# Kernel optimization log

Hardware: AMD Instinct MI355X
Metric: run time of the kernel (lower is better)

## Reference

```python
import jax, jax.numpy as jnp
import numpy as np

N = 50000      # total atoms in batched graph
E = 800000     # edges
IN = 128       # in_feats
OUT = 64       # out_feats (per GAT head)
H = 4          # num_heads
NEG_SLOPE = 0.2
BN_EPS = 1e-5


def setup_inputs() -> dict:
    key = jax.random.key(0)
    ks = jax.random.split(key, 16)
    s = 0.1  # keep activations well-scaled
    return {
        "node_feats": jax.random.normal(ks[0], (N, IN), jnp.float32),
        "W_fc":       jax.random.normal(ks[1], (IN, H * OUT), jnp.float32) * s,
        "attn_l":     jax.random.normal(ks[2], (H, OUT), jnp.float32) * s,
        "attn_r":     jax.random.normal(ks[3], (H, OUT), jnp.float32) * s,
        "gat_res_w":  jax.random.normal(ks[4], (IN, H * OUT), jnp.float32) * s,
        "gat_bias":   jax.random.normal(ks[5], (H * OUT,), jnp.float32) * s,
        "conv_w":     jax.random.normal(ks[6], (1, H, 1), jnp.float32) * s,
        "conv_b":     jax.random.normal(ks[7], (1,), jnp.float32) * s,
        "res_w":      jax.random.normal(ks[8], (IN, OUT), jnp.float32) * s,
        "res_b":      jax.random.normal(ks[9], (OUT,), jnp.float32) * s,
        "bn_gamma":   jnp.ones((OUT,), jnp.float32),
        "bn_beta":    jnp.zeros((OUT,), jnp.float32),
        "src":        jax.random.randint(ks[10], (E,), 0, N, jnp.int32),
        "dst":        jax.random.randint(ks[11], (E,), 0, N, jnp.int32),
        "etype":      0,
    }


def reference(node_feats, W_fc, attn_l, attn_r, gat_res_w, gat_bias,
              conv_w, conv_b, res_w, res_b, bn_gamma, bn_beta,
              src, dst, etype):
    # ---- GATConv (DGL semantics, eval mode: no dropout) ----
    h = (node_feats @ W_fc).reshape(-1, H, OUT)            # [N,H,D]
    el = jnp.sum(h * attn_l, axis=-1)                      # [N,H]
    er = jnp.sum(h * attn_r, axis=-1)                      # [N,H]
    e = jax.nn.leaky_relu(el[src] + er[dst], NEG_SLOPE)    # [E,H]
    # segment softmax over incoming edges of each dst node
    m = jax.ops.segment_max(e, dst, num_segments=N)        # [N,H]
    m = jnp.where(jnp.isfinite(m), m, 0.0)                 # empty segments
    a = jnp.exp(e - m[dst])                                # [E,H]
    ssum = jax.ops.segment_sum(a, dst, num_segments=N)     # [N,H]
    alpha = a / (ssum[dst] + 1e-16)                        # [E,H]
    # weighted aggregation: rst[v] = sum_{(u->v)} alpha * h[u]
    rst = jax.ops.segment_sum(alpha[:, :, None] * h[src], dst, num_segments=N)  # [N,H,D]
    # GAT residual (in != H*OUT -> linear res_fc, no bias) + bias + activation
    rst = rst + (node_feats @ gat_res_w).reshape(-1, H, OUT) + gat_bias.reshape(H, OUT)
    rst = jax.nn.relu(rst)                                 # [N,H,D]
    # ---- Conv1d(4 -> 1, kernel=1): weighted head merge ----
    y = jnp.einsum("nhd,h->nd", rst, conv_w[0, :, 0]) + conv_b[0]  # [N,D]
    # ---- outer residual ----
    y = y + jax.nn.relu(node_feats @ res_w + res_b)
    # ---- BatchNorm1d (training-style batch stats) ----
    mean = jnp.mean(y, axis=0)
    var = jnp.var(y, axis=0)
    return (y - mean) / jnp.sqrt(var + BN_EPS) * bn_gamma + bn_beta
```

## Files before the change

### kernel.cpp

```cpp
#include <hip/hip_runtime.h>

#define IN_F   128
#define OUTD   64
#define HOUT   256
#define NEG_SLOPE 0.2f
#define BN_EPS 1e-5f
#define HISTB  256

typedef __attribute__((ext_vector_type(8))) short bf16x8;
typedef __attribute__((ext_vector_type(4))) float f32x4;
typedef __attribute__((ext_vector_type(2))) float f32x2;

__device__ __forceinline__ unsigned short f2bf(float f) {
    union { float f; unsigned u; } v; v.f = f;
    unsigned r = (v.u + 0x7FFF + ((v.u >> 16) & 1)) >> 16;
    return (unsigned short)r;
}
__device__ __forceinline__ float bf2f(unsigned short h) {
    union { unsigned u; float f; } v; v.u = ((unsigned)h) << 16;
    return v.f;
}
__device__ __forceinline__ float u2f(unsigned u) {
    union { unsigned u; float f; } v; v.u = u;
    return v.f;
}
__device__ __forceinline__ unsigned f2u(float f) {
    union { float f; unsigned u; } v; v.f = f;
    return v.u;
}

__device__ __forceinline__ int b2idx(int c, int k) {
    int tt, j;
    if (c < 256)      { tt = (c >> 4) & 3;                     j = c >> 6; }
    else if (c < 512) { int cc = c - 256; tt = 4 + ((cc >> 4) & 3); j = cc >> 6; }
    else if (c < 576) { int cc = c - 512; tt = 8;              j = cc >> 4; }
    else              { tt = 9;                                j = 0; }
    int n15 = c & 15;
    int ks = k >> 5, qd = (k >> 3) & 3, kk = k & 7;
    return ((((tt * 4 + j) * 4 + ks) * 64) + qd * 16 + n15) * 8 + kk;
}

__global__ __launch_bounds__(256) void k0_pack(
    const float* __restrict__ W_fc, const float* __restrict__ W_gres,
    const float* __restrict__ W_res,
    const float* __restrict__ attn_l, const float* __restrict__ attn_r,
    unsigned short* __restrict__ Btg2)
{
    int bid = blockIdx.x, t = threadIdx.x;
    if (bid < 288) {
        int idx = bid * 256 + t;
        int c = idx >> 7, k = idx & 127;
        float v;
        if (c < 256)      v = W_fc[k * HOUT + c];
        else if (c < 512) v = W_gres[k * HOUT + (c - 256)];
        else              v = W_res[k * OUTD + (c - 512)];
        Btg2[b2idx(c, k)] = f2bf(v);
        return;
    }
    for (int p = t; p < 512; p += 256) {
        int h = p >> 7, k = p & 127;
        float sl = 0.f, sr = 0.f;
        for (int d = 0; d < 64; ++d) {
            float wv = W_fc[k * HOUT + h * 64 + d];
            sl += wv * attn_l[h * 64 + d];
            sr += wv * attn_r[h * 64 + d];
        }
        Btg2[b2idx(576 + h, k)] = f2bf(sl);
        Btg2[b2idx(580 + h, k)] = f2bf(sr);
    }
    for (int p = t; p < 8 * 128; p += 256) {
        int c = 584 + (p >> 7), k = p & 127;
        Btg2[b2idx(c, k)] = 0;
    }
}

__global__ __launch_bounds__(256) void k1_gemm(
    const float* __restrict__ A, const unsigned short* __restrict__ Btg2,
    const float* __restrict__ gat_bias, const float* __restrict__ res_b,
    const int* __restrict__ dst, int* __restrict__ degree, int* __restrict__ rank,
    unsigned char* __restrict__ Hh8, unsigned char* __restrict__ Hr8,
    unsigned short* __restrict__ Rres,
    float* __restrict__ el, float* __restrict__ er,
    int N, int E, int Gblocks)
{
    int t = threadIdx.x;

    if (blockIdx.x >= Gblocks) {
        int ht = (blockIdx.x - Gblocks) * 256 + t;
        for (int e = ht; e < E; e += HISTB * 256)
            rank[e] = atomicAdd(degree + dst[e], 1);
        return;
    }

    int w = t >> 6, lane = t & 63, quad = lane >> 4, n15 = lane & 15;
    int gw = blockIdx.x * 4 + w;
    int T = (N + 15) / 16;
    if (gw >= T) return;

    int m0 = gw * 16;
    bool full = (m0 + 16 <= N);
    int lofs = (quad * 16 + n15) * 8;

    bf16x8 af[4];
    {
        int r = m0 + n15;
#pragma unroll
        for (int ks = 0; ks < 4; ++ks) {
            float4 v0 = make_float4(0.f, 0.f, 0.f, 0.f), v1 = v0;
            if (r < N) {
                const float* ap = A + (size_t)r * IN_F + ks * 32 + quad * 8;
                v0 = *(const float4*)ap;
                v1 = *(const float4*)(ap + 4);
            }
            bf16x8 o;
            o[0] = f2bf(v0.x); o[1] = f2bf(v0.y); o[2] = f2bf(v0.z); o[3] = f2bf(v0.w);
            o[4] = f2bf(v1.x); o[5] = f2bf(v1.y); o[6] = f2bf(v1.z); o[7] = f2bf(v1.w);
            af[ks] = o;
        }
    }

#pragma unroll
    for (int s = 0; s < 4; ++s) {
        f32x4 acc[4] = {};
#pragma unroll
        for (int ks = 0; ks < 4; ++ks) {
            bf16x8 bfr[4];
#pragma unroll
            for (int j = 0; j < 4; ++j)
                bfr[j] = *(const bf16x8*)(Btg2 + ((s * 16 + j * 4 + ks) << 9) + lofs);
#pragma unroll
            for (int j = 0; j < 4; ++j)
                acc[j] = __builtin_amdgcn_mfma_f32_16x16x32_bf16(af[ks], bfr[j], acc[j], 0, 0, 0);
        }
#pragma unroll
        for (int reg = 0; reg < 4; ++reg) {
            int r = m0 + quad * 4 + reg;
            if (full || r < N) {
                unsigned pk = (unsigned)__builtin_amdgcn_cvt_pk_fp8_f32(acc[0][reg], acc[1][reg], 0, false);
                pk = (unsigned)__builtin_amdgcn_cvt_pk_fp8_f32(acc[2][reg], acc[3][reg], (int)pk, true);
                *(unsigned*)(Hh8 + ((size_t)r << 8) + (s * 16 + n15) * 4) = pk;
            }
        }
    }

#pragma unroll
    for (int s = 0; s < 4; ++s) {
        f32x4 acc[4] = {};
#pragma unroll
        for (int ks = 0; ks < 4; ++ks) {
            bf16x8 bfr[4];
#pragma unroll
            for (int j = 0; j < 4; ++j)
                bfr[j] = *(const bf16x8*)(Btg2 + (((4 + s) * 16 + j * 4 + ks) << 9) + lofs);
#pragma unroll
            for (int j = 0; j < 4; ++j)
                acc[j] = __builtin_amdgcn_mfma_f32_16x16x32_bf16(af[ks], bfr[j], acc[j], 0, 0, 0);
        }
        float b0 = gat_bias[0 * 64 + s * 16 + n15];
        float b1 = gat_bias[1 * 64 + s * 16 + n15];
        float b2 = gat_bias[2 * 64 + s * 16 + n15];
        float b3 = gat_bias[3 * 64 + s * 16 + n15];
#pragma unroll
        for (int reg = 0; reg < 4; ++reg) {
            int r = m0 + quad * 4 + reg;
            if (full || r < N) {
                unsigned pk = (unsigned)__builtin_amdgcn_cvt_pk_fp8_f32(acc[0][reg] + b0, acc[1][reg] + b1, 0, false);
                pk = (unsigned)__builtin_amdgcn_cvt_pk_fp8_f32(acc[2][reg] + b2, acc[3][reg] + b3, (int)pk, true);
                *(unsigned*)(Hr8 + ((size_t)r << 8) + (s * 16 + n15) * 4) = pk;
            }
        }
    }

    {
        f32x4 acc[4] = {};
#pragma unroll
        for (int ks = 0; ks < 4; ++ks) {
            bf16x8 bfr[4];
#pragma unroll
            for (int j = 0; j < 4; ++j)
                bfr[j] = *(const bf16x8*)(Btg2 + ((8 * 16 + j * 4 + ks) << 9) + lofs);
#pragma unroll
            for (int j = 0; j < 4; ++j)
                acc[j] = __builtin_amdgcn_mfma_f32_16x16x32_bf16(af[ks], bfr[j], acc[j], 0, 0, 0);
        }
#pragma unroll
        for (int reg = 0; reg < 4; ++reg) {
            int r = m0 + quad * 4 + reg;
            if (full || r < N) {
#pragma unroll
                for (int j = 0; j < 4; ++j)
                    Rres[(size_t)r * OUTD + j * 16 + n15] = f2bf(acc[j][reg] + res_b[j * 16 + n15]);
            }
        }
    }

    {
        f32x4 acc2 = {};
#pragma unroll
        for (int ks = 0; ks < 4; ++ks) {
            bf16x8 b = *(const bf16x8*)(Btg2 + ((9 * 16 + ks) << 9) + lofs);
            acc2 = __builtin_amdgcn_mfma_f32_16x16x32_bf16(af[ks], b, acc2, 0, 0, 0);
        }
#pragma unroll
        for (int reg = 0; reg < 4; ++reg) {
            int r = m0 + quad * 4 + reg;
            if ((full || r < N) && n15 < 8) {
                float v = acc2[reg];
                if (n15 < 4) el[(size_t)r * 4 + n15] = v;
                else         er[(size_t)r * 4 + (n15 - 4)] = v;
            }
        }
    }
}

__global__ __launch_bounds__(256) void scanA_kernel(const int* __restrict__ degree,
                                                    int* __restrict__ excl,
                                                    int* __restrict__ blocksum, int N) {
    __shared__ int sm[256];
    int t = threadIdx.x;
    int i = blockIdx.x * 256 + t;
    int d = (i < N) ? degree[i] : 0;
    sm[t] = d; __syncthreads();
    for (int off = 1; off < 256; off <<= 1) {
        int v = (t >= off) ? sm[t - off] : 0;
        __syncthreads();
        sm[t] += v;
        __syncthreads();
    }
    if (i < N) excl[i] = sm[t] - d;
    if (t == 255) blocksum[blockIdx.x] = sm[255];
}

__global__ __launch_bounds__(256) void scatter_kernel(
    const int* __restrict__ src, const int* __restrict__ dst,
    const int* __restrict__ rank, const int* __restrict__ excl,
    const int* __restrict__ blocksum, int* __restrict__ base,
    unsigned* __restrict__ usrc_sorted, int E, int nb) {
    __shared__ int sm[256];
    __shared__ int base_lds[256];
    int t = threadIdx.x;
    int d0 = (t < nb) ? blocksum[t] : 0;
    sm[t] = d0; __syncthreads();
    for (int off = 1; off < 256; off <<= 1) {
        int v = (t >= off) ? sm[t - off] : 0;
        __syncthreads();
        sm[t] += v;
        __syncthreads();
    }
    base_lds[t] = sm[t] - d0;
    if (blockIdx.x == 0) base[t] = sm[t] - d0;
    __syncthreads();

    int e = blockIdx.x * 256 + t;
    if (e >= E) return;
    int d = dst[e];
    int p = excl[d] + base_lds[d >> 8] + rank[e];
    usrc_sorted[p] = (unsigned)src[e] << 8;
}

__global__ __launch_bounds__(256) void agg_kernel(
    const unsigned char* __restrict__ Hh8, const unsigned char* __restrict__ Hr8,
    const unsigned short* __restrict__ Rres, const float* __restrict__ el,
    const float* __restrict__ er,
    const int* __restrict__ excl, const int* __restrict__ base,
    const unsigned* __restrict__ usrc_sorted,
    const float* __restrict__ conv_w, const float* __restrict__ conv_b,
    float* __restrict__ y, float* __restrict__ bnsum8, float* __restrict__ bnsq8,
    int N, int E)
{
    __shared__ float smem[256];
    __shared__ float smem2[256];
    int t = threadIdx.x;
    int wave = t >> 6, lane = t & 63;
    int v = blockIdx.x * 4 + wave;

    float yv = 0.f;
    if (v < N) {
        int b  = excl[v] + base[v >> 8];
        int e2 = (v + 1 < N) ? (excl[v + 1] + base[(v + 1) >> 8]) : E;
        int deg = e2 - b;

        float4 rv = *(const float4*)(er + (size_t)v * 4);
        const unsigned char* hbase = Hh8 + lane * 4;
        float a0 = 0.f, a1 = 0.f, a2 = 0.f, a3 = 0.f;
        float p0 = 0.f, p1 = 0.f, p2 = 0.f, p3 = 0.f;

        for (int i0 = 0; i0 < deg; i0 += 64) {
            int j = i0 + lane;
            unsigned ux = 0;
            float s0 = 0.f, s1 = 0.f, s2 = 0.f, s3 = 0.f;
            if (j < deg) {
                ux = usrc_sorted[b + j];
                float4 l = *(const float4*)(el + ((size_t)(ux >> 8)) * 4);
                float x;
                x = l.x + rv.x; x = x > 0.f ? x : NEG_SLOPE * x; s0 = __expf(x);
                x = l.y + rv.y; x = x > 0.f ? x : NEG_SLOPE * x; s1 = __expf(x);
                x = l.z + rv.z; x = x > 0.f ? x : NEG_SLOPE * x; s2 = __expf(x);
                x = l.w + rv.w; x = x > 0.f ? x : NEG_SLOPE * x; s3 = __expf(x);
                p0 += s0; p1 += s1; p2 += s2; p3 += s3;
            }
            int cl = deg - i0; if (cl > 64) cl = 64;
            int jj = 0;
            for (; jj + 3 < cl; jj += 4) {
                unsigned u_[4], hv[4];
                float w0[4], w1[4], w2[4], w3[4];
#pragma unroll
                for (int k = 0; k < 4; ++k) {
                    u_[k] = (unsigned)__builtin_amdgcn_readlane((int)ux, jj + k);
                    w0[k] = u2f((unsigned)__builtin_amdgcn_readlane((int)f2u(s0), jj + k));
                    w1[k] = u2f((unsigned)__builtin_amdgcn_readlane((int)f2u(s1), jj + k));
                    w2[k] = u2f((unsigned)__builtin_amdgcn_readlane((int)f2u(s2), jj + k));
                    w3[k] = u2f((unsigned)__builtin_amdgcn_readlane((int)f2u(s3), jj + k));
                }
#pragma unroll
                for (int k = 0; k < 4; ++k)
                    hv[k] = *(const unsigned*)(hbase + u_[k]);
#pragma unroll
                for (int k = 0; k < 4; ++k) {
                    f32x2 lo = __builtin_amdgcn_cvt_pk_f32_fp8(hv[k], false);
                    f32x2 hi = __builtin_amdgcn_cvt_pk_f32_fp8(hv[k], true);
                    a0 += w0[k] * lo.x;
                    a1 += w1[k] * lo.y;
                    a2 += w2[k] * hi.x;
                    a3 += w3[k] * hi.y;
                }
            }
            for (; jj < cl; ++jj) {
                unsigned uA = (unsigned)__builtin_amdgcn_readlane((int)ux, jj);
                float w0 = u2f((unsigned)__builtin_amdgcn_readlane((int)f2u(s0), jj));
                float w1 = u2f((unsigned)__builtin_amdgcn_readlane((int)f2u(s1), jj));
                float w2 = u2f((unsigned)__builtin_amdgcn_readlane((int)f2u(s2), jj));
                float w3 = u2f((unsigned)__builtin_amdgcn_readlane((int)f2u(s3), jj));
                unsigned hvA = *(const unsigned*)(hbase + uA);
                f32x2 lo = __builtin_amdgcn_cvt_pk_f32_fp8(hvA, false);
                f32x2 hi = __builtin_amdgcn_cvt_pk_f32_fp8(hvA, true);
                a0 += w0 * lo.x;
                a1 += w1 * lo.y;
                a2 += w2 * hi.x;
                a3 += w3 * hi.y;
            }
        }
#pragma unroll
        for (int off = 1; off < 64; off <<= 1) {
            p0 += __shfl_xor(p0, off); p1 += __shfl_xor(p1, off);
            p2 += __shfl_xor(p2, off); p3 += __shfl_xor(p3, off);
        }
        float r0 = 1.f / (p0 + 1e-16f), r1 = 1.f / (p1 + 1e-16f);
        float r2 = 1.f / (p2 + 1e-16f), r3 = 1.f / (p3 + 1e-16f);

        unsigned hr = *(const unsigned*)(Hr8 + ((size_t)v << 8) + lane * 4);
        f32x2 rlo = __builtin_amdgcn_cvt_pk_f32_fp8(hr, false);
        f32x2 rhi = __builtin_amdgcn_cvt_pk_f32_fp8(hr, true);
        float resv = bf2f(Rres[(size_t)v * OUTD + lane]);
        yv = conv_b[0] + (resv > 0.f ? resv : 0.f);
        float tt;
        tt = a0 * r0 + rlo.x; tt = tt > 0.f ? tt : 0.f; yv += conv_w[0] * tt;
        tt = a1 * r1 + rlo.y; tt = tt > 0.f ? tt : 0.f; yv += conv_w[1] * tt;
        tt = a2 * r2 + rhi.x; tt = tt > 0.f ? tt : 0.f; yv += conv_w[2] * tt;
        tt = a3 * r3 + rhi.y; tt = tt > 0.f ? tt : 0.f; yv += conv_w[3] * tt;
        y[(size_t)v * OUTD + lane] = yv;
    }

    smem[t] = yv;
    smem2[t] = yv * yv;
    __syncthreads();
    if (t < 64) {
        float s = smem[t] + smem[t + 64] + smem[t + 128] + smem[t + 192];
        float q = smem2[t] + smem2[t + 64] + smem2[t + 128] + smem2[t + 192];
        int c = (blockIdx.x & 7) << 6;
        atomicAdd(bnsum8 + c + t, s);
        atomicAdd(bnsq8 + c + t, q);
    }
}

__global__ __launch_bounds__(256) void norm_kernel(
    const float* __restrict__ y,
    const float* __restrict__ bnsum8, const float* __restrict__ bnsq8,
    const float* __restrict__ gamma, const float* __restrict__ beta,
    float* __restrict__ out, int total4, float invN) {
    __shared__ float scale[64], shift[64];
    int t = threadIdx.x;
    if (t < 64) {
        float s = 0.f, q = 0.f;
#pragma unroll
        for (int c = 0; c < 8; ++c) { s += bnsum8[c * 64 + t]; q += bnsq8[c * 64 + t]; }
        float mean = s * invN;
        float var = q * invN - mean * mean;
        float sc = gamma[t] * rsqrtf(var + BN_EPS);
        scale[t] = sc;
        shift[t] = beta[t] - mean * sc;
    }
    __syncthreads();
    int idx = blockIdx.x * blockDim.x + t;
    if (idx >= total4) return;
    float4 v = *(const float4*)(y + (size_t)idx * 4);
    int d = (idx * 4) & 63;
    float4 o;
    o.x = v.x * scale[d + 0] + shift[d + 0];
    o.y = v.y * scale[d + 1] + shift[d + 1];
    o.z = v.z * scale[d + 2] + shift[d + 2];
    o.w = v.w * scale[d + 3] + shift[d + 3];
    *(float4*)(out + (size_t)idx * 4) = o;
}

extern "C" void kernel_launch(void* const* d_in, const int* in_sizes, int n_in,
                              void* d_out, int out_size, void* d_ws, size_t ws_size,
                              hipStream_t stream) {
    const float* node_feats = (const float*)d_in[0];
    const float* W_fc       = (const float*)d_in[1];
    const float* attn_l     = (const float*)d_in[2];
    const float* attn_r     = (const float*)d_in[3];
    const float* gat_res_w  = (const float*)d_in[4];
    const float* gat_bias   = (const float*)d_in[5];
    const float* conv_w     = (const float*)d_in[6];
    const float* conv_b     = (const float*)d_in[7];
    const float* res_w      = (const float*)d_in[8];
    const float* res_b      = (const float*)d_in[9];
    const float* bn_gamma   = (const float*)d_in[10];
    const float* bn_beta    = (const float*)d_in[11];
    const int*   src        = (const int*)d_in[12];
    const int*   dst        = (const int*)d_in[13];

    const int N = in_sizes[0] / IN_F;
    const int E = in_sizes[12];
    const int nb = (N + 255) / 256;
    const int T = (N + 15) / 16;
    const int Gblocks = (T + 3) / 4;

    char* ws = (char*)d_ws;
    size_t off = 0;
    auto alloc = [&](size_t bytes) -> void* {
        void* p = (void*)(ws + off);
        off += (bytes + 255) & ~(size_t)255;
        return p;
    };

    int*   degree  = (int*)alloc((size_t)N * 4);
    float* bnsum8  = (float*)alloc(8 * 64 * 4);
    float* bnsq8   = (float*)alloc(8 * 64 * 4);
    size_t zero_bytes = off;
    int*            rank        = (int*)alloc((size_t)E * 4);
    int*            excl        = (int*)alloc((size_t)N * 4);
    int*            blocksum    = (int*)alloc(256 * 4);
    int*            base        = (int*)alloc(256 * 4);
    unsigned*       usrc_sorted = (unsigned*)alloc((size_t)E * 4);
    unsigned short* Btg2        = (unsigned short*)alloc((size_t)10 * 16 * 512 * 2);
    unsigned char*  Hh8         = (unsigned char*)alloc((size_t)N * 256);
    unsigned char*  Hr8         = (unsigned char*)alloc((size_t)N * 256);
    unsigned short* Rres        = (unsigned short*)alloc((size_t)N * OUTD * 2);
    float*          el          = (float*)alloc((size_t)N * 4 * 4);
    float*          er          = (float*)alloc((size_t)N * 4 * 4);
    float*          y           = (float*)alloc((size_t)N * OUTD * 4);
    (void)ws_size; (void)n_in; (void)out_size;

    hipMemsetAsync(d_ws, 0, zero_bytes, stream);

    k0_pack<<<289, 256, 0, stream>>>(W_fc, gat_res_w, res_w, attn_l, attn_r, Btg2);
    k1_gemm<<<Gblocks + HISTB, 256, 0, stream>>>(node_feats, Btg2, gat_bias, res_b,
                                                 dst, degree, rank, Hh8, Hr8, Rres,
                                                 el, er, N, E, Gblocks);
    scanA_kernel<<<nb, 256, 0, stream>>>(degree, excl, blocksum, N);
    scatter_kernel<<<(E + 255) / 256, 256, 0, stream>>>(src, dst, rank, excl, blocksum,
                                                        base, usrc_sorted, E, nb);
    agg_kernel<<<(N + 3) / 4, 256, 0, stream>>>(Hh8, Hr8, Rres, el, er, excl, base,
                                                usrc_sorted, conv_w, conv_b, y,
                                                bnsum8, bnsq8, N, E);
    norm_kernel<<<(N * OUTD / 4 + 255) / 256, 256, 0, stream>>>(y, bnsum8, bnsq8,
                                                                bn_gamma, bn_beta, (float*)d_out,
                                                                N * OUTD / 4, 1.f / (float)N);
}
```

Baseline: 222.2 us.

## Move degree histogram into pack kernel and fuse scatter into GEMM launch

The degree-histogram atomics move from the GEMM kernel into the weight-pack kernel. The scan now runs before the GEMM, so the edge scatter (CSR fill) can run as extra blocks of the GEMM launch instead of as a separate kernel. This removes one launch and overlaps the scatter's memory traffic with the MFMA work. The GEMM inner loops also load all B fragments for a stripe before issuing the MFMAs, which raises register use for more memory-level parallelism.

```diff
diff --git a/kernel.cpp b/kernel.cpp
--- a/kernel.cpp
+++ b/kernel.cpp
@@ -5,7 +5,8 @@
 #define HOUT   256
 #define NEG_SLOPE 0.2f
 #define BN_EPS 1e-5f
-#define HISTB  256
+#define HB     1024
+#define SB     512
 
 typedef __attribute__((ext_vector_type(8))) short bf16x8;
 typedef __attribute__((ext_vector_type(4))) float f32x4;
@@ -44,7 +45,9 @@
     const float* __restrict__ W_fc, const float* __restrict__ W_gres,
     const float* __restrict__ W_res,
     const float* __restrict__ attn_l, const float* __restrict__ attn_r,
-    unsigned short* __restrict__ Btg2)
+    unsigned short* __restrict__ Btg2,
+    const int* __restrict__ dst, int* __restrict__ degree,
+    int* __restrict__ rank, int E)
 {
     int bid = blockIdx.x, t = threadIdx.x;
     if (bid < 288) {
@@ -57,38 +60,63 @@
         Btg2[b2idx(c, k)] = f2bf(v);
         return;
     }
-    for (int p = t; p < 512; p += 256) {
-        int h = p >> 7, k = p & 127;
-        float sl = 0.f, sr = 0.f;
-        for (int d = 0; d < 64; ++d) {
-            float wv = W_fc[k * HOUT + h * 64 + d];
-            sl += wv * attn_l[h * 64 + d];
-            sr += wv * attn_r[h * 64 + d];
-        }
-        Btg2[b2idx(576 + h, k)] = f2bf(sl);
-        Btg2[b2idx(580 + h, k)] = f2bf(sr);
-    }
-    for (int p = t; p < 8 * 128; p += 256) {
-        int c = 584 + (p >> 7), k = p & 127;
-        Btg2[b2idx(c, k)] = 0;
-    }
+    if (bid == 288) {
+        for (int p = t; p < 512; p += 256) {
+            int h = p >> 7, k = p & 127;
+            float sl = 0.f, sr = 0.f;
+            for (int d = 0; d < 64; ++d) {
+                float wv = W_fc[k * HOUT + h * 64 + d];
+                sl += wv * attn_l[h * 64 + d];
+                sr += wv * attn_r[h * 64 + d];
+            }
+            Btg2[b2idx(576 + h, k)] = f2bf(sl);
+            Btg2[b2idx(580 + h, k)] = f2bf(sr);
+        }
+        for (int p = t; p < 8 * 128; p += 256) {
+            int c = 584 + (p >> 7), k = p & 127;
+            Btg2[b2idx(c, k)] = 0;
+        }
+        return;
+    }
+    int ht = (bid - 289) * 256 + t;
+    for (int e = ht; e < E; e += HB * 256)
+        rank[e] = atomicAdd(degree + dst[e], 1);
 }
 
 __global__ __launch_bounds__(256) void k1_gemm(
     const float* __restrict__ A, const unsigned short* __restrict__ Btg2,
     const float* __restrict__ gat_bias, const float* __restrict__ res_b,
-    const int* __restrict__ dst, int* __restrict__ degree, int* __restrict__ rank,
+    const int* __restrict__ src, const int* __restrict__ dst,
+    const int* __restrict__ rank, const int* __restrict__ excl,
+    const int* __restrict__ blocksum, int* __restrict__ base,
+    unsigned* __restrict__ usrc_sorted,
     unsigned char* __restrict__ Hh8, unsigned char* __restrict__ Hr8,
     unsigned short* __restrict__ Rres,
     float* __restrict__ el, float* __restrict__ er,
-    int N, int E, int Gblocks)
+    int N, int E, int Gblocks, int nb)
 {
     int t = threadIdx.x;
 
     if (blockIdx.x >= Gblocks) {
-        int ht = (blockIdx.x - Gblocks) * 256 + t;
-        for (int e = ht; e < E; e += HISTB * 256)
-            rank[e] = atomicAdd(degree + dst[e], 1);
+        __shared__ int sm[256];
+        __shared__ int base_lds[256];
+        int sb = blockIdx.x - Gblocks;
+        int d0 = (t < nb) ? blocksum[t] : 0;
+        sm[t] = d0; __syncthreads();
+        for (int off = 1; off < 256; off <<= 1) {
+            int v = (t >= off) ? sm[t - off] : 0;
+            __syncthreads();
+            sm[t] += v;
+            __syncthreads();
+        }
+        base_lds[t] = sm[t] - d0;
+        if (sb == 0) base[t] = sm[t] - d0;
+        __syncthreads();
+        for (int e = sb * 256 + t; e < E; e += SB * 256) {
+            int d = dst[e];
+            int p = excl[d] + base_lds[d >> 8] + rank[e];
+            usrc_sorted[p] = (unsigned)src[e] << 8;
+        }
         return;
     }
 
@@ -121,17 +149,18 @@
 
 #pragma unroll
     for (int s = 0; s < 4; ++s) {
+        bf16x8 bfr[4][4];
+#pragma unroll
+        for (int ks = 0; ks < 4; ++ks)
+#pragma unroll
+            for (int j = 0; j < 4; ++j)
+                bfr[ks][j] = *(const bf16x8*)(Btg2 + ((s * 16 + j * 4 + ks) << 9) + lofs);
         f32x4 acc[4] = {};
 #pragma unroll
-        for (int ks = 0; ks < 4; ++ks) {
-            bf16x8 bfr[4];
-#pragma unroll
-            for (int j = 0; j < 4; ++j)
-                bfr[j] = *(const bf16x8*)(Btg2 + ((s * 16 + j * 4 + ks) << 9) + lofs);
-#pragma unroll
-            for (int j = 0; j < 4; ++j)
-                acc[j] = __builtin_amdgcn_mfma_f32_16x16x32_bf16(af[ks], bfr[j], acc[j], 0, 0, 0);
-        }
+        for (int ks = 0; ks < 4; ++ks)
+#pragma unroll
+            for (int j = 0; j < 4; ++j)
+                acc[j] = __builtin_amdgcn_mfma_f32_16x16x32_bf16(af[ks], bfr[ks][j], acc[j], 0, 0, 0);
 #pragma unroll
         for (int reg = 0; reg < 4; ++reg) {
             int r = m0 + quad * 4 + reg;
@@ -145,17 +174,18 @@
 
 #pragma unroll
     for (int s = 0; s < 4; ++s) {
+        bf16x8 bfr[4][4];
+#pragma unroll
+        for (int ks = 0; ks < 4; ++ks)
+#pragma unroll
+            for (int j = 0; j < 4; ++j)
+                bfr[ks][j] = *(const bf16x8*)(Btg2 + (((4 + s) * 16 + j * 4 + ks) << 9) + lofs);
         f32x4 acc[4] = {};
 #pragma unroll
-        for (int ks = 0; ks < 4; ++ks) {
-            bf16x8 bfr[4];
-#pragma unroll
-            for (int j = 0; j < 4; ++j)
-                bfr[j] = *(const bf16x8*)(Btg2 + (((4 + s) * 16 + j * 4 + ks) << 9) + lofs);
-#pragma unroll
-            for (int j = 0; j < 4; ++j)
-                acc[j] = __builtin_amdgcn_mfma_f32_16x16x32_bf16(af[ks], bfr[j], acc[j], 0, 0, 0);
-        }
+        for (int ks = 0; ks < 4; ++ks)
+#pragma unroll
+            for (int j = 0; j < 4; ++j)
+                acc[j] = __builtin_amdgcn_mfma_f32_16x16x32_bf16(af[ks], bfr[ks][j], acc[j], 0, 0, 0);
         float b0 = gat_bias[0 * 64 + s * 16 + n15];
         float b1 = gat_bias[1 * 64 + s * 16 + n15];
         float b2 = gat_bias[2 * 64 + s * 16 + n15];
@@ -172,17 +202,18 @@
     }
 
     {
+        bf16x8 bfr[4][4];
+#pragma unroll
+        for (int ks = 0; ks < 4; ++ks)
+#pragma unroll
+            for (int j = 0; j < 4; ++j)
+                bfr[ks][j] = *(const bf16x8*)(Btg2 + ((8 * 16 + j * 4 + ks) << 9) + lofs);
         f32x4 acc[4] = {};
 #pragma unroll
-        for (int ks = 0; ks < 4; ++ks) {
-            bf16x8 bfr[4];
-#pragma unroll
-            for (int j = 0; j < 4; ++j)
-                bfr[j] = *(const bf16x8*)(Btg2 + ((8 * 16 + j * 4 + ks) << 9) + lofs);
-#pragma unroll
-            for (int j = 0; j < 4; ++j)
-                acc[j] = __builtin_amdgcn_mfma_f32_16x16x32_bf16(af[ks], bfr[j], acc[j], 0, 0, 0);
-        }
+        for (int ks = 0; ks < 4; ++ks)
+#pragma unroll
+            for (int j = 0; j < 4; ++j)
+                acc[j] = __builtin_amdgcn_mfma_f32_16x16x32_bf16(af[ks], bfr[ks][j], acc[j], 0, 0, 0);
 #pragma unroll
         for (int reg = 0; reg < 4; ++reg) {
             int r = m0 + quad * 4 + reg;
@@ -195,12 +226,14 @@
     }
 
     {
+        bf16x8 b4[4];
+#pragma unroll
+        for (int ks = 0; ks < 4; ++ks)
+            b4[ks] = *(const bf16x8*)(Btg2 + ((9 * 16 + ks) << 9) + lofs);
         f32x4 acc2 = {};
 #pragma unroll
-        for (int ks = 0; ks < 4; ++ks) {
-            bf16x8 b = *(const bf16x8*)(Btg2 + ((9 * 16 + ks) << 9) + lofs);
-            acc2 = __builtin_amdgcn_mfma_f32_16x16x32_bf16(af[ks], b, acc2, 0, 0, 0);
-        }
+        for (int ks = 0; ks < 4; ++ks)
+            acc2 = __builtin_amdgcn_mfma_f32_16x16x32_bf16(af[ks], b4[ks], acc2, 0, 0, 0);
 #pragma unroll
         for (int reg = 0; reg < 4; ++reg) {
             int r = m0 + quad * 4 + reg;
@@ -229,33 +262,6 @@
     }
     if (i < N) excl[i] = sm[t] - d;
     if (t == 255) blocksum[blockIdx.x] = sm[255];
-}
-
-__global__ __launch_bounds__(256) void scatter_kernel(
-    const int* __restrict__ src, const int* __restrict__ dst,
-    const int* __restrict__ rank, const int* __restrict__ excl,
-    const int* __restrict__ blocksum, int* __restrict__ base,
-    unsigned* __restrict__ usrc_sorted, int E, int nb) {
-    __shared__ int sm[256];
-    __shared__ int base_lds[256];
-    int t = threadIdx.x;
-    int d0 = (t < nb) ? blocksum[t] : 0;
-    sm[t] = d0; __syncthreads();
-    for (int off = 1; off < 256; off <<= 1) {
-        int v = (t >= off) ? sm[t - off] : 0;
-        __syncthreads();
-        sm[t] += v;
-        __syncthreads();
-    }
-    base_lds[t] = sm[t] - d0;
-    if (blockIdx.x == 0) base[t] = sm[t] - d0;
-    __syncthreads();
-
-    int e = blockIdx.x * 256 + t;
-    if (e >= E) return;
-    int d = dst[e];
-    int p = excl[d] + base_lds[d >> 8] + rank[e];
-    usrc_sorted[p] = (unsigned)src[e] << 8;
 }
 
 __global__ __launch_bounds__(256) void agg_kernel(
@@ -455,13 +461,13 @@
 
     hipMemsetAsync(d_ws, 0, zero_bytes, stream);
 
-    k0_pack<<<289, 256, 0, stream>>>(W_fc, gat_res_w, res_w, attn_l, attn_r, Btg2);
-    k1_gemm<<<Gblocks + HISTB, 256, 0, stream>>>(node_feats, Btg2, gat_bias, res_b,
-                                                 dst, degree, rank, Hh8, Hr8, Rres,
-                                                 el, er, N, E, Gblocks);
+    k0_pack<<<289 + HB, 256, 0, stream>>>(W_fc, gat_res_w, res_w, attn_l, attn_r, Btg2,
+                                          dst, degree, rank, E);
     scanA_kernel<<<nb, 256, 0, stream>>>(degree, excl, blocksum, N);
-    scatter_kernel<<<(E + 255) / 256, 256, 0, stream>>>(src, dst, rank, excl, blocksum,
-                                                        base, usrc_sorted, E, nb);
+    k1_gemm<<<Gblocks + SB, 256, 0, stream>>>(node_feats, Btg2, gat_bias, res_b,
+                                              src, dst, rank, excl, blocksum, base,
+                                              usrc_sorted, Hh8, Hr8, Rres,
+                                              el, er, N, E, Gblocks, nb);
     agg_kernel<<<(N + 3) / 4, 256, 0, stream>>>(Hh8, Hr8, Rres, el, er, excl, base,
                                                 usrc_sorted, conv_w, conv_b, y,
                                                 bnsum8, bnsq8, N, E);
```

New measurement: 226.9 us. 2.1% more time.

## Stage GEMM weight tiles in LDS with double buffering and 64-row warp tiles

Applied to the files above, without the earlier changes.

The node-feature GEMM kernel now gives each warp 64 rows (four 16-row MFMA tiles) instead of 16, so every B fragment read is reused across four A tiles. The weight matrix is copied into a double-buffered shared-memory tile with global_load_lds, and the next 16 KB tile is prefetched while the current one feeds the MFMAs. This is meant to cut repeated global and L2 reads of the packed weights. In exchange the GEMM launches about a quarter as many blocks, which lowers parallelism on a wide GPU. Every block, including the histogram blocks, now reserves 32 KB of LDS, and the last staged tile reads a full 16 KB that may extend past the packed weight data.

```diff
diff --git a/kernel.cpp b/kernel.cpp
--- a/kernel.cpp
+++ b/kernel.cpp
@@ -27,6 +27,13 @@
 __device__ __forceinline__ unsigned f2u(float f) {
     union { float f; unsigned u; } v; v.f = f;
     return v.u;
+}
+
+__device__ __forceinline__ void stage16(const void* g, void* l) {
+    __builtin_amdgcn_global_load_lds(
+        (const __attribute__((address_space(1))) unsigned int*)g,
+        (__attribute__((address_space(3))) unsigned int*)l,
+        16, 0, 0);
 }
 
 __device__ __forceinline__ int b2idx(int c, int k) {
@@ -83,6 +90,7 @@
     float* __restrict__ el, float* __restrict__ er,
     int N, int E, int Gblocks)
 {
+    __shared__ short ldsB[2][8192];
     int t = threadIdx.x;
 
     if (blockIdx.x >= Gblocks) {
@@ -93,123 +101,122 @@
     }
 
     int w = t >> 6, lane = t & 63, quad = lane >> 4, n15 = lane & 15;
-    int gw = blockIdx.x * 4 + w;
-    int T = (N + 15) / 16;
-    if (gw >= T) return;
-
-    int m0 = gw * 16;
-    bool full = (m0 + 16 <= N);
-    int lofs = (quad * 16 + n15) * 8;
-
-    bf16x8 af[4];
+    int base = blockIdx.x * 256 + w * 64;
+    bool active = (base < N);
+    int lofs2 = (quad * 16 + n15) * 16;
+
+    bf16x8 af[4][4];
+    if (active) {
+#pragma unroll
+        for (int mi = 0; mi < 4; ++mi) {
+            int r = base + mi * 16 + n15;
+#pragma unroll
+            for (int ks = 0; ks < 4; ++ks) {
+                float4 v0 = make_float4(0.f, 0.f, 0.f, 0.f), v1 = v0;
+                if (r < N) {
+                    const float* ap = A + (size_t)r * IN_F + ks * 32 + quad * 8;
+                    v0 = *(const float4*)ap;
+                    v1 = *(const float4*)(ap + 4);
+                }
+                bf16x8 o;
+                o[0] = f2bf(v0.x); o[1] = f2bf(v0.y); o[2] = f2bf(v0.z); o[3] = f2bf(v0.w);
+                o[4] = f2bf(v1.x); o[5] = f2bf(v1.y); o[6] = f2bf(v1.z); o[7] = f2bf(v1.w);
+                af[mi][ks] = o;
+            }
+        }
+    }
+
     {
-        int r = m0 + n15;
-#pragma unroll
-        for (int ks = 0; ks < 4; ++ks) {
-            float4 v0 = make_float4(0.f, 0.f, 0.f, 0.f), v1 = v0;
-            if (r < N) {
-                const float* ap = A + (size_t)r * IN_F + ks * 32 + quad * 8;
-                v0 = *(const float4*)ap;
-                v1 = *(const float4*)(ap + 4);
-            }
-            bf16x8 o;
-            o[0] = f2bf(v0.x); o[1] = f2bf(v0.y); o[2] = f2bf(v0.z); o[3] = f2bf(v0.w);
-            o[4] = f2bf(v1.x); o[5] = f2bf(v1.y); o[6] = f2bf(v1.z); o[7] = f2bf(v1.w);
-            af[ks] = o;
-        }
-    }
-
-#pragma unroll
-    for (int s = 0; s < 4; ++s) {
-        f32x4 acc[4] = {};
-#pragma unroll
-        for (int ks = 0; ks < 4; ++ks) {
-            bf16x8 bfr[4];
-#pragma unroll
-            for (int j = 0; j < 4; ++j)
-                bfr[j] = *(const bf16x8*)(Btg2 + ((s * 16 + j * 4 + ks) << 9) + lofs);
-#pragma unroll
-            for (int j = 0; j < 4; ++j)
-                acc[j] = __builtin_amdgcn_mfma_f32_16x16x32_bf16(af[ks], bfr[j], acc[j], 0, 0, 0);
-        }
-#pragma unroll
-        for (int reg = 0; reg < 4; ++reg) {
-            int r = m0 + quad * 4 + reg;
-            if (full || r < N) {
-                unsigned pk = (unsigned)__builtin_amdgcn_cvt_pk_fp8_f32(acc[0][reg], acc[1][reg], 0, false);
-                pk = (unsigned)__builtin_amdgcn_cvt_pk_fp8_f32(acc[2][reg], acc[3][reg], (int)pk, true);
-                *(unsigned*)(Hh8 + ((size_t)r << 8) + (s * 16 + n15) * 4) = pk;
-            }
-        }
-    }
-
-#pragma unroll
-    for (int s = 0; s < 4; ++s) {
-        f32x4 acc[4] = {};
-#pragma unroll
-        for (int ks = 0; ks < 4; ++ks) {
-            bf16x8 bfr[4];
-#pragma unroll
-            for (int j = 0; j < 4; ++j)
-                bfr[j] = *(const bf16x8*)(Btg2 + (((4 + s) * 16 + j * 4 + ks) << 9) + lofs);
-#pragma unroll
-            for (int j = 0; j < 4; ++j)
-                acc[j] = __builtin_amdgcn_mfma_f32_16x16x32_bf16(af[ks], bfr[j], acc[j], 0, 0, 0);
-        }
-        float b0 = gat_bias[0 * 64 + s * 16 + n15];
-        float b1 = gat_bias[1 * 64 + s * 16 + n15];
-        float b2 = gat_bias[2 * 64 + s * 16 + n15];
-        float b3 = gat_bias[3 * 64 + s * 16 + n15];
-#pragma unroll
-        for (int reg = 0; reg < 4; ++reg) {
-            int r = m0 + quad * 4 + reg;
-            if (full || r < N) {
-                unsigned pk = (unsigned)__builtin_amdgcn_cvt_pk_fp8_f32(acc[0][reg] + b0, acc[1][reg] + b1, 0, false);
-                pk = (unsigned)__builtin_amdgcn_cvt_pk_fp8_f32(acc[2][reg] + b2, acc[3][reg] + b3, (int)pk, true);
-                *(unsigned*)(Hr8 + ((size_t)r << 8) + (s * 16 + n15) * 4) = pk;
-            }
-        }
-    }
-
-    {
-        f32x4 acc[4] = {};
-#pragma unroll
-        for (int ks = 0; ks < 4; ++ks) {
-            bf16x8 bfr[4];
-#pragma unroll
-            for (int j = 0; j < 4; ++j)
-                bfr[j] = *(const bf16x8*)(Btg2 + ((8 * 16 + j * 4 + ks) << 9) + lofs);
-#pragma unroll
-            for (int j = 0; j < 4; ++j)
-                acc[j] = __builtin_amdgcn_mfma_f32_16x16x32_bf16(af[ks], bfr[j], acc[j], 0, 0, 0);
-        }
-#pragma unroll
-        for (int reg = 0; reg < 4; ++reg) {
-            int r = m0 + quad * 4 + reg;
-            if (full || r < N) {
-#pragma unroll
-                for (int j = 0; j < 4; ++j)
-                    Rres[(size_t)r * OUTD + j * 16 + n15] = f2bf(acc[j][reg] + res_b[j * 16 + n15]);
-            }
-        }
-    }
-
-    {
-        f32x4 acc2 = {};
-#pragma unroll
-        for (int ks = 0; ks < 4; ++ks) {
-            bf16x8 b = *(const bf16x8*)(Btg2 + ((9 * 16 + ks) << 9) + lofs);
-            acc2 = __builtin_amdgcn_mfma_f32_16x16x32_bf16(af[ks], b, acc2, 0, 0, 0);
-        }
-#pragma unroll
-        for (int reg = 0; reg < 4; ++reg) {
-            int r = m0 + quad * 4 + reg;
-            if ((full || r < N) && n15 < 8) {
-                float v = acc2[reg];
-                if (n15 < 4) el[(size_t)r * 4 + n15] = v;
-                else         er[(size_t)r * 4 + (n15 - 4)] = v;
-            }
-        }
+        const char* gb = (const char*)Btg2;
+#pragma unroll
+        for (int c = 0; c < 4; ++c) {
+            int ch = w * 4 + c;
+            stage16(gb + ch * 1024 + lane * 16, (char*)&ldsB[0][0] + ch * 1024);
+        }
+    }
+    __syncthreads();
+
+    for (int tt = 0; tt < 10; ++tt) {
+        int cur = tt & 1;
+        if (tt + 1 < 10) {
+            const char* gb = (const char*)Btg2 + (size_t)(tt + 1) * 16384;
+#pragma unroll
+            for (int c = 0; c < 4; ++c) {
+                int ch = w * 4 + c;
+                stage16(gb + ch * 1024 + lane * 16, (char*)&ldsB[cur ^ 1][0] + ch * 1024);
+            }
+        }
+        if (active) {
+            f32x4 acc[4][4] = {};
+#pragma unroll
+            for (int j = 0; j < 4; ++j) {
+                bf16x8 bj[4];
+#pragma unroll
+                for (int ks = 0; ks < 4; ++ks)
+                    bj[ks] = *(const bf16x8*)((const char*)&ldsB[cur][0] + (j * 4 + ks) * 1024 + lofs2);
+#pragma unroll
+                for (int ks = 0; ks < 4; ++ks)
+#pragma unroll
+                    for (int mi = 0; mi < 4; ++mi)
+                        acc[mi][j] = __builtin_amdgcn_mfma_f32_16x16x32_bf16(af[mi][ks], bj[ks], acc[mi][j], 0, 0, 0);
+            }
+            if (tt < 4) {
+                int s = tt;
+#pragma unroll
+                for (int mi = 0; mi < 4; ++mi)
+#pragma unroll
+                    for (int reg = 0; reg < 4; ++reg) {
+                        int r = base + mi * 16 + quad * 4 + reg;
+                        if (r < N) {
+                            unsigned pk = (unsigned)__builtin_amdgcn_cvt_pk_fp8_f32(acc[mi][0][reg], acc[mi][1][reg], 0, false);
+                            pk = (unsigned)__builtin_amdgcn_cvt_pk_fp8_f32(acc[mi][2][reg], acc[mi][3][reg], (int)pk, true);
+                            *(unsigned*)(Hh8 + ((size_t)r << 8) + (s * 16 + n15) * 4) = pk;
+                        }
+                    }
+            } else if (tt < 8) {
+                int s = tt - 4;
+                float b0 = gat_bias[0 * 64 + s * 16 + n15];
+                float b1 = gat_bias[1 * 64 + s * 16 + n15];
+                float b2 = gat_bias[2 * 64 + s * 16 + n15];
+                float b3 = gat_bias[3 * 64 + s * 16 + n15];
+#pragma unroll
+                for (int mi = 0; mi < 4; ++mi)
+#pragma unroll
+                    for (int reg = 0; reg < 4; ++reg) {
+                        int r = base + mi * 16 + quad * 4 + reg;
+                        if (r < N) {
+                            unsigned pk = (unsigned)__builtin_amdgcn_cvt_pk_fp8_f32(acc[mi][0][reg] + b0, acc[mi][1][reg] + b1, 0, false);
+                            pk = (unsigned)__builtin_amdgcn_cvt_pk_fp8_f32(acc[mi][2][reg] + b2, acc[mi][3][reg] + b3, (int)pk, true);
+                            *(unsigned*)(Hr8 + ((size_t)r << 8) + (s * 16 + n15) * 4) = pk;
+                        }
+                    }
+            } else if (tt == 8) {
+#pragma unroll
+                for (int mi = 0; mi < 4; ++mi)
+#pragma unroll
+                    for (int reg = 0; reg < 4; ++reg) {
+                        int r = base + mi * 16 + quad * 4 + reg;
+                        if (r < N) {
+#pragma unroll
+                            for (int j = 0; j < 4; ++j)
+                                Rres[(size_t)r * OUTD + j * 16 + n15] = f2bf(acc[mi][j][reg] + res_b[j * 16 + n15]);
+                        }
+                    }
+            } else {
+#pragma unroll
+                for (int mi = 0; mi < 4; ++mi)
+#pragma unroll
+                    for (int reg = 0; reg < 4; ++reg) {
+                        int r = base + mi * 16 + quad * 4 + reg;
+                        if (r < N && n15 < 8) {
+                            float v = acc[mi][0][reg];
+                            if (n15 < 4) el[(size_t)r * 4 + n15] = v;
+                            else         er[(size_t)r * 4 + (n15 - 4)] = v;
+                        }
+                    }
+            }
+        }
+        __syncthreads();
     }
 }
 
@@ -424,8 +431,7 @@
     const int N = in_sizes[0] / IN_F;
     const int E = in_sizes[12];
     const int nb = (N + 255) / 256;
-    const int T = (N + 15) / 16;
-    const int Gblocks = (T + 3) / 4;
+    const int Gblocks = (N + 255) / 256;
 
     char* ws = (char*)d_ws;
     size_t off = 0;
```

New measurement: 232.0 us. 1.04x slower.
